# Optimization experiments

Measured on AMD Instinct MI355X. Metric: run time of the kernel, lower is better.

Reference implementation:

```python
import jax, jax.numpy as jnp
import numpy as np

HIDDEN = 4096
NUM_HEADS = 32
NUM_KV_HEADS = 8
HEAD_DIM = 128
T = 2048
ROPE_THETA = 10000.0


def setup_inputs() -> dict:
    key = jax.random.key(0)
    ks = jax.random.split(key, 10)
    s = 0.02
    return {
        "hidden_states": jax.random.normal(ks[0], (T, HIDDEN), dtype=jnp.float32),
        "positions": jnp.arange(T, dtype=jnp.int32),
        "Wq": jax.random.normal(ks[1], (NUM_HEADS * HEAD_DIM, HIDDEN), dtype=jnp.float32) * s,
        "bq": jax.random.normal(ks[2], (NUM_HEADS * HEAD_DIM,), dtype=jnp.float32) * s,
        "Wk": jax.random.normal(ks[3], (NUM_KV_HEADS * HEAD_DIM, HIDDEN), dtype=jnp.float32) * s,
        "bk": jax.random.normal(ks[4], (NUM_KV_HEADS * HEAD_DIM,), dtype=jnp.float32) * s,
        "Wv": jax.random.normal(ks[5], (NUM_KV_HEADS * HEAD_DIM, HIDDEN), dtype=jnp.float32) * s,
        "bv": jax.random.normal(ks[6], (NUM_KV_HEADS * HEAD_DIM,), dtype=jnp.float32) * s,
        "Wo": jax.random.normal(ks[7], (HIDDEN, HIDDEN), dtype=jnp.float32) * s,
        "bo": jax.random.normal(ks[8], (HIDDEN,), dtype=jnp.float32) * s,
    }


def _rope_cos_sin(positions, head_dim, base):
    # neox-style rotary over the full head_dim
    half = head_dim // 2
    inv_freq = 1.0 / (base ** (jnp.arange(0, half, dtype=jnp.float32) * 2.0 / head_dim))
    angles = positions.astype(jnp.float32)[:, None] * inv_freq[None, :]  # [T, half]
    return jnp.cos(angles), jnp.sin(angles)


def _apply_rope(x, cos, sin):
    # x: [T, H, D]; neox: split halves, rotate
    half = x.shape[-1] // 2
    x1, x2 = x[..., :half], x[..., half:]
    c = cos[:, None, :]
    s = sin[:, None, :]
    return jnp.concatenate([x1 * c - x2 * s, x2 * c + x1 * s], axis=-1)


def reference(hidden_states, positions, Wq, bq, Wk, bk, Wv, bv, Wo, bo):
    q = (hidden_states @ Wq.T + bq).reshape(T, NUM_HEADS, HEAD_DIM)
    k = (hidden_states @ Wk.T + bk).reshape(T, NUM_KV_HEADS, HEAD_DIM)
    v = (hidden_states @ Wv.T + bv).reshape(T, NUM_KV_HEADS, HEAD_DIM)

    cos, sin = _rope_cos_sin(positions, HEAD_DIM, ROPE_THETA)
    q = _apply_rope(q, cos, sin)
    k = _apply_rope(k, cos, sin)

    scale = 1.0 / np.sqrt(HEAD_DIM).astype(np.float32)
    group = NUM_HEADS // NUM_KV_HEADS
    qg = q.reshape(T, NUM_KV_HEADS, group, HEAD_DIM)
    # scores: [g_kv, r, q, k] without materializing repeated KV heads
    scores = jnp.einsum('qgrd,kgd->grqk', qg, k) * scale
    causal = positions[:, None] >= positions[None, :]  # [T, T]
    scores = jnp.where(causal[None, None], scores, jnp.finfo(scores.dtype).min)
    probs = jax.nn.softmax(scores, axis=-1)
    o = jnp.einsum('grqk,kgd->qgrd', probs, v).reshape(T, NUM_HEADS * HEAD_DIM)
    return o @ Wo.T + bo
```

## Files before the change

### kernel.cpp

```cpp
#include <hip/hip_runtime.h>
#include <stdint.h>

typedef unsigned short u16;
typedef __bf16 bf16x8_t __attribute__((ext_vector_type(8)));
typedef float f32x4_t __attribute__((ext_vector_type(4)));

#define T_SEQ 2048
#define HID 4096
#define ROWQKV 6144

__device__ __forceinline__ float bf2f(u16 x){ return __uint_as_float(((uint32_t)x)<<16); }
__device__ __forceinline__ u16 f2bf(float f){
  uint32_t u = __float_as_uint(f);
  return (u16)((u + 0x7fffu + ((u>>16)&1u)) >> 16);
}

__device__ __forceinline__ void gload16(const void* g, void* l){
  __builtin_amdgcn_global_load_lds(
      (const __attribute__((address_space(1))) uint32_t*)g,
      (__attribute__((address_space(3))) uint32_t*)l, 16, 0, 0);
}

__device__ __forceinline__ uint32_t cvtpk(float lo, float hi_){
  uint32_t r;
  asm("v_cvt_pk_bf16_f32 %0, %1, %2" : "=v"(r) : "v"(lo), "v"(hi_));
  return r;
}

__global__ void cvt_kernel(const float* __restrict__ src, u16* __restrict__ dst, int n8){
  int i = blockIdx.x*blockDim.x + threadIdx.x;
  if (i >= n8) return;
  const float4* s = (const float4*)src;
  float4 a = s[2*i], b = s[2*i+1];
  union { u16 u[8]; uint4 v; } o;
  o.u[0]=f2bf(a.x); o.u[1]=f2bf(a.y); o.u[2]=f2bf(a.z); o.u[3]=f2bf(a.w);
  o.u[4]=f2bf(b.x); o.u[5]=f2bf(b.y); o.u[6]=f2bf(b.z); o.u[7]=f2bf(b.w);
  ((uint4*)dst)[i] = o.v;
}

__global__ void setup_kernel(const float* __restrict__ bq, const float* __restrict__ bk,
                             const float* __restrict__ bv, const int* __restrict__ pos,
                             float* __restrict__ bqkv, float* __restrict__ cost,
                             float* __restrict__ sint){
  int i = blockIdx.x*blockDim.x + threadIdx.x;
  if (i < 6144) bqkv[i] = (i<4096) ? bq[i] : ((i<5120) ? bk[i-4096] : bv[i-5120]);
  if (i < T_SEQ*64){
    int t = i >> 6, d = i & 63;
    float inv = powf(10000.0f, -(float)(2*d) / 128.0f);
    float ang = (float)pos[t] * inv;
    cost[i] = cosf(ang);
    sint[i] = sinf(ang);
  }
}

#define GBAR __builtin_amdgcn_s_barrier()
#define LGKM0 do{ asm volatile("s_waitcnt lgkmcnt(0)" ::: "memory"); \
                  __builtin_amdgcn_sched_barrier(0); }while(0)

#define BUF6 28672

#define AREAD6(mh, ck) do{ \
  const u16* ab = &lds[cur + aoff + (mh)*4096]; \
  afr[0] = *(const bf16x8_t*)&ab[0*1024 + (ck)]; \
  afr[1] = *(const bf16x8_t*)&ab[1*1024 + (ck)]; \
  afr[2] = *(const bf16x8_t*)&ab[2*1024 + (ck)]; \
  afr[3] = *(const bf16x8_t*)&ab[3*1024 + (ck)]; }while(0)

#define BREAD6(ck) do{ \
  const u16* bb = &lds[cur + boff]; \
  bfr[0] = *(const bf16x8_t*)&bb[0*1024 + (ck)]; \
  bfr[1] = *(const bf16x8_t*)&bb[1*1024 + (ck)]; \
  bfr[2] = *(const bf16x8_t*)&bb[2*1024 + (ck)]; }while(0)

#define MM12(mh) do{ \
  _Pragma("unroll") \
  for (int mi=0; mi<4; ++mi){ \
    _Pragma("unroll") \
    for (int n=0; n<3; ++n) \
      acc[(mh)*4+mi][n] = __builtin_amdgcn_mfma_f32_16x16x32_bf16(afr[mi], bfr[n], acc[(mh)*4+mi][n],0,0,0); \
  } }while(0)

__global__ __launch_bounds__(512, 2)
void gemm_qkv(const u16* __restrict__ A, const u16* __restrict__ B,
              const float* __restrict__ bias, u16* __restrict__ Cb,
              int K, int N)
{
  __shared__ u16 lds[2*BUF6];
  const int tid = threadIdx.x, lane = tid & 63, w = tid >> 6;
  const int l15 = lane & 15, l4 = lane >> 4;
  const int wm = w >> 2, wn = w & 3;

  const int nwg = gridDim.x * gridDim.y;
  int flat = blockIdx.y * gridDim.x + blockIdx.x;
  flat = (flat & 7) * (nwg >> 3) + (flat >> 3);
  const int bx = flat % gridDim.x, by = flat / gridDim.x;
  const int bm = by * 256, bn = bx * 192;

  const int srow = w*8 + (lane >> 3);
  const int swc  = ((lane & 7) ^ (lane >> 3)) * 8;
  const u16* pA = A + (size_t)(bm + srow)*K + swc;
  const u16* pB = B + (size_t)(bn + srow)*K + swc;
  const size_t j64 = (size_t)64*K;
  const int wu = w*512;

  const int cA0 = ((0 + l4) ^ (l15 & 7)) * 8;
  const int cA1 = ((4 + l4) ^ (l15 & 7)) * 8;
  const int aoff = (wm*128 + l15) * 64;
  const int boff = 16384 + (wn*48 + l15) * 64;

  f32x4_t acc[8][3] = {};
  const int KT = K >> 6;

  gload16(pA + 0*j64, &lds[0     + wu]);
  gload16(pA + 1*j64, &lds[4096  + wu]);
  gload16(pA + 2*j64, &lds[8192  + wu]);
  gload16(pA + 3*j64, &lds[12288 + wu]);
  gload16(pB + 0*j64, &lds[16384 + wu]);
  gload16(pB + 1*j64, &lds[20480 + wu]);
  gload16(pB + 2*j64, &lds[24576 + wu]);
  pA += 64; pB += 64;
  asm volatile("s_waitcnt vmcnt(0)" ::: "memory");
  GBAR;

  for (int t = 0; t < KT; ++t){
    const int cur = (t & 1) * BUF6;
    const int nxt = ((t + 1) & 1) * BUF6;
    const bool st = (t + 1 < KT);
    bf16x8_t afr[4], bfr[3];

    BREAD6(cA0); AREAD6(0, cA0);
    if (st){
      gload16(pA + 0*j64, &lds[nxt + 0     + wu]);
      gload16(pA + 1*j64, &lds[nxt + 4096  + wu]);
      gload16(pA + 2*j64, &lds[nxt + 8192  + wu]);
      gload16(pA + 3*j64, &lds[nxt + 12288 + wu]);
    }
    GBAR; LGKM0;
    __builtin_amdgcn_s_setprio(1); MM12(0); __builtin_amdgcn_s_setprio(0);
    GBAR;

    AREAD6(1, cA0);
    if (st){
      gload16(pB + 0*j64, &lds[nxt + 16384 + wu]);
      gload16(pB + 1*j64, &lds[nxt + 20480 + wu]);
      gload16(pB + 2*j64, &lds[nxt + 24576 + wu]);
      pA += 64; pB += 64;
    }
    GBAR; LGKM0;
    __builtin_amdgcn_s_setprio(1); MM12(1); __builtin_amdgcn_s_setprio(0);
    GBAR;

    BREAD6(cA1); AREAD6(0, cA1);
    GBAR; LGKM0;
    __builtin_amdgcn_s_setprio(1); MM12(0); __builtin_amdgcn_s_setprio(0);
    GBAR;

    AREAD6(1, cA1);
    GBAR; LGKM0;
    __builtin_amdgcn_s_setprio(1); MM12(1); __builtin_amdgcn_s_setprio(0);
    if (st) asm volatile("s_waitcnt vmcnt(0)" ::: "memory");
    GBAR;
  }

  #pragma unroll
  for (int m=0;m<8;m++){
    #pragma unroll
    for (int n=0;n<3;n++){
      #pragma unroll
      for (int j=0;j<4;j++){
        int row = bm + wm*128 + (m>>2)*64 + (m&3)*16 + l4*4 + j;
        int col = bn + wn*48 + n*16 + l15;
        Cb[(size_t)row*N + col] = f2bf(acc[m][n][j] + bias[col]);
      }
    }
  }
}

#define BUFK 24576

#define KMREAD(ck) do{ \
  afr[0] = *(const bf16x8_t*)&lds[cur + aoff + 0*1024 + (ck)]; \
  afr[1] = *(const bf16x8_t*)&lds[cur + aoff + 1*1024 + (ck)]; \
  afr[2] = *(const bf16x8_t*)&lds[cur + aoff + 2*1024 + (ck)]; \
  afr[3] = *(const bf16x8_t*)&lds[cur + aoff + 3*1024 + (ck)]; \
  bfr[0] = *(const bf16x8_t*)&lds[cur + boff + 0*1024 + (ck)]; \
  bfr[1] = *(const bf16x8_t*)&lds[cur + boff + 1*1024 + (ck)]; \
  bfr[2] = *(const bf16x8_t*)&lds[cur + boff + 2*1024 + (ck)]; \
  bfr[3] = *(const bf16x8_t*)&lds[cur + boff + 3*1024 + (ck)]; }while(0)

#define MM16KM do{ \
  _Pragma("unroll") \
  for (int mi=0; mi<4; ++mi){ \
    _Pragma("unroll") \
    for (int n=0; n<4; ++n) \
      acc[mi][n] = __builtin_amdgcn_mfma_f32_16x16x32_bf16(afr[mi], bfr[n], acc[mi][n],0,0,0); \
  } }while(0)

__global__ __launch_bounds__(512, 2)
void gemm_km(const u16* __restrict__ A, const u16* __restrict__ B,
             const float* __restrict__ bias, float* __restrict__ Cf,
             int K, int N)
{
  __shared__ u16 lds[3*BUFK];
  const int tid = threadIdx.x, lane = tid & 63, w = tid >> 6;
  const int l15 = lane & 15, l4 = lane >> 4;
  const int wm = w >> 1, wn = w & 1;

  const int nwg = gridDim.x * gridDim.y;
  int flat = blockIdx.y * gridDim.x + blockIdx.x;
  flat = (flat & 7) * (nwg >> 3) + (flat >> 3);
  const int bx = flat % gridDim.x, by = flat / gridDim.x;
  const int bm = by * 256, bn = bx * 128;

  const int srow = w*8 + (lane >> 3);
  const int swc  = ((lane & 7) ^ (lane >> 3)) * 8;
  const u16* pA = A + (size_t)(bm + srow)*K + swc;
  const u16* pB = B + (size_t)(bn + srow)*K + swc;
  const size_t j64 = (size_t)64*K;
  const int wu = w*512;

  const int cA0 = ((0 + l4) ^ (l15 & 7)) * 8;
  const int cA1 = ((4 + l4) ^ (l15 & 7)) * 8;
  const int aoff = (wm*64 + l15) * 64;
  const int boff = 16384 + (wn*64 + l15) * 64;

  f32x4_t acc[4][4] = {};
  const int KT = K >> 6;

  gload16(pA + 0*j64,      &lds[0*4096 + wu]);
  gload16(pA + 1*j64,      &lds[1*4096 + wu]);
  gload16(pA + 2*j64,      &lds[2*4096 + wu]);
  gload16(pA + 3*j64,      &lds[3*4096 + wu]);
  gload16(pB + 0*j64,      &lds[16384 + 0*4096 + wu]);
  gload16(pB + 1*j64,      &lds[16384 + 1*4096 + wu]);
  gload16(pA + 64 + 0*j64, &lds[BUFK + 0*4096 + wu]);
  gload16(pA + 64 + 1*j64, &lds[BUFK + 1*4096 + wu]);
  gload16(pA + 64 + 2*j64, &lds[BUFK + 2*4096 + wu]);
  gload16(pA + 64 + 3*j64, &lds[BUFK + 3*4096 + wu]);
  gload16(pB + 64 + 0*j64, &lds[BUFK + 16384 + 0*4096 + wu]);
  gload16(pB + 64 + 1*j64, &lds[BUFK + 16384 + 1*4096 + wu]);
  pA += 128; pB += 128;
  asm volatile("s_waitcnt vmcnt(6)" ::: "memory");
  GBAR;

  for (int t = 0; t < KT; ++t){
    const int cur = (t % 3) * BUFK;
    const int sb  = ((t + 2) % 3) * BUFK;
    const bool st = (t + 2 < KT);
    bf16x8_t afr[4], bfr[4];

    KMREAD(cA0);
    if (st){
      gload16(pA + 0*j64, &lds[sb + 0*4096 + wu]);
      gload16(pA + 1*j64, &lds[sb + 1*4096 + wu]);
      gload16(pA + 2*j64, &lds[sb + 2*4096 + wu]);
    }
    GBAR; LGKM0;
    __builtin_amdgcn_s_setprio(1); MM16KM; __builtin_amdgcn_s_setprio(0);
    GBAR;

    KMREAD(cA1);
    if (st){
      gload16(pA + 3*j64, &lds[sb + 3*4096 + wu]);
      gload16(pB + 0*j64, &lds[sb + 16384 + 0*4096 + wu]);
      gload16(pB + 1*j64, &lds[sb + 16384 + 1*4096 + wu]);
      pA += 64; pB += 64;
    }
    GBAR; LGKM0;
    __builtin_amdgcn_s_setprio(1); MM16KM; __builtin_amdgcn_s_setprio(0);
    if (st)              asm volatile("s_waitcnt vmcnt(6)" ::: "memory");
    else if (t + 1 < KT) asm volatile("s_waitcnt vmcnt(0)" ::: "memory");
    GBAR;
  }

  #pragma unroll
  for (int mi=0;mi<4;mi++){
    #pragma unroll
    for (int n=0;n<4;n++){
      #pragma unroll
      for (int j=0;j<4;j++){
        int row = bm + wm*64 + mi*16 + l4*4 + j;
        int col = bn + wn*64 + n*16 + l15;
        Cf[(size_t)row*N + col] = acc[mi][n][j] + bias[col];
      }
    }
  }
}

__global__ void rope_kernel(u16* __restrict__ qkv, const float* __restrict__ cost,
                            const float* __restrict__ sint){
  int i = blockIdx.x*blockDim.x + threadIdx.x;
  int t = i / 2560;
  int r = i % 2560;
  int h = r >> 6, d = r & 63;
  int base = (h < 32) ? h*128 : (4096 + (h-32)*128);
  size_t p1 = (size_t)t*ROWQKV + base + d;
  float x1 = bf2f(qkv[p1]), x2 = bf2f(qkv[p1+64]);
  float c = cost[(t<<6)+d], s = sint[(t<<6)+d];
  qkv[p1]    = f2bf(x1*c - x2*s);
  qkv[p1+64] = f2bf(x2*c + x1*s);
}

#define VOFF 16384
#define POFF 25600

__global__ __launch_bounds__(256, 2)
void attn_kernel(const u16* __restrict__ qkv, u16* __restrict__ attn_o)
{
  __shared__ u16 lds[29696];
  const int tid = threadIdx.x, lane = tid&63, wid = tid>>6;
  const int l15 = lane&15, l4 = lane>>4;
  const int l7 = l15 & 7;
  const int h  = blockIdx.x & 31;
  const int qt = 31 - (blockIdx.x >> 5);
  const int q0 = qt * 64;
  const int kvh = h >> 2;
  const u16* Qg = qkv + h*128;
  const u16* Kg = qkv + 4096 + kvh*128;
  const u16* Vg = qkv + 5120 + kvh*128;
  const float c2 = 0.127543147f;

  bf16x8_t qf[4];
  {
    size_t qrow = (size_t)(q0 + wid*16 + l15);
    #pragma unroll
    for (int kk=0;kk<4;kk++)
      qf[kk] = *(const bf16x8_t*)(Qg + qrow*ROWQKV + kk*32 + l4*8);
  }
  float mrow[4] = {-1e30f,-1e30f,-1e30f,-1e30f};
  f32x4_t oacc[9] = {};

  const u16* ksrc[4];
  int kls[4];
  #pragma unroll
  for (int i=0;i<4;i++){
    const int c = wid*4 + i;
    ksrc[i] = Kg + (size_t)((c&7)*8 + (lane>>3))*ROWQKV
               + (c>>3)*64 + ((lane&7)^(lane>>3))*8;
    kls[i] = c*512;
  }
  const int kvp = tid & 31;
  const int vd0 = (tid >> 5) * 16;
  uint4 rv[4];

  #pragma unroll
  for (int i=0;i<4;i++) gload16(ksrc[i], &lds[kls[i]]);
  #pragma unroll
  for (int i=0;i<4;i++) ksrc[i] += (size_t)64*ROWQKV;
  {
    const u16* va = Vg + (size_t)(2*kvp)*ROWQKV + vd0;
    rv[0] = *(const uint4*)va;            rv[1] = *(const uint4*)(va + 8);
    rv[2] = *(const uint4*)(va + ROWQKV); rv[3] = *(const uint4*)(va + ROWQKV + 8);
    *(uint32_t*)&lds[24576 + tid*4]     = 0x3F803F80u;
    *(uint32_t*)&lds[24576 + tid*4 + 2] = 0x3F803F80u;
  }
  __syncthreads();
  {
    const u16* ra = (const u16*)&rv[0]; const u16* rb = (const u16*)&rv[2];
    #pragma unroll
    for (int e=0;e<8;e++)
      *(uint32_t*)&lds[VOFF + (vd0+e)*64 + ((kvp>>2)^(e&7))*8 + 2*(kvp&3)]
          = (uint32_t)ra[e] | ((uint32_t)rb[e] << 16);
    ra = (const u16*)&rv[1]; rb = (const u16*)&rv[3];
    #pragma unroll
    for (int e=0;e<8;e++)
      *(uint32_t*)&lds[VOFF + (vd0+8+e)*64 + ((kvp>>2)^(e&7))*8 + 2*(kvp&3)]
          = (uint32_t)ra[e] | ((uint32_t)rb[e] << 16);
  }
  __syncthreads();

  for (int kt = 0; kt <= qt; ++kt){
    const int kv0 = kt * 64;
    const int kcur = (kt & 1) * 8192;
    const bool pre = (kt < qt);
    if (pre){
      const int knxt = ((kt+1) & 1) * 8192;
      #pragma unroll
      for (int i=0;i<4;i++) gload16(ksrc[i], &lds[knxt + kls[i]]);
      #pragma unroll
      for (int i=0;i<4;i++) ksrc[i] += (size_t)64*ROWQKV;
      const u16* va = Vg + (size_t)(kv0 + 64 + 2*kvp)*ROWQKV + vd0;
      rv[0] = *(const uint4*)va;            rv[1] = *(const uint4*)(va + 8);
      rv[2] = *(const uint4*)(va + ROWQKV); rv[3] = *(const uint4*)(va + ROWQKV + 8);
    }

    f32x4_t sacc[4] = {};
    __builtin_amdgcn_s_setprio(1);
    #pragma unroll
    for (int n=0;n<4;n++){
      #pragma unroll
      for (int kk=0;kk<4;kk++){
        bf16x8_t kf = *(const bf16x8_t*)&lds[kcur + (kk>>1)*4096
                        + (n*16+l15)*64 + (((kk&1)*4 + l4) ^ l7)*8];
        sacc[n] = __builtin_amdgcn_mfma_f32_16x16x32_bf16(qf[kk], kf, sacc[n], 0,0,0);
      }
    }
    __builtin_amdgcn_s_setprio(0);
    float sv[4][4];
    float pmax[4] = {-1e30f,-1e30f,-1e30f,-1e30f};
    bool diag = (kt == qt);
    #pragma unroll
    for (int n=0;n<4;n++){
      int kvcol = kv0 + n*16 + l15;
      #pragma unroll
      for (int j=0;j<4;j++){
        float s = sacc[n][j];
        int qrow = q0 + wid*16 + l4*4 + j;
        if (diag && kvcol > qrow) s = -1e30f;
        sv[n][j] = s;
        pmax[j] = fmaxf(pmax[j], s);
      }
    }
    #pragma unroll
    for (int off=1; off<16; off<<=1){
      #pragma unroll
      for (int j=0;j<4;j++)
        pmax[j] = fmaxf(pmax[j], __shfl_xor(pmax[j], off, 64));
    }
    float esc[4], mc[4];
    #pragma unroll
    for (int j=0;j<4;j++){
      float mn = fmaxf(mrow[j], pmax[j]);
      esc[j] = exp2f((mrow[j] - mn) * c2);
      mrow[j] = mn;
      mc[j] = mn * c2;
    }
    #pragma unroll
    for (int n=0;n<4;n++){
      #pragma unroll
      for (int j=0;j<4;j++)
        sv[n][j] = exp2f(fmaf(sv[n][j], c2, -mc[j]));
    }
    #pragma unroll
    for (int n=0;n<9;n++){
      #pragma unroll
      for (int j=0;j<4;j++) oacc[n][j] *= esc[j];
    }
    {
      const int r0 = wid*16 + l4*4;
      #pragma unroll
      for (int n=0;n<4;n++){
        uint32_t p01 = cvtpk(sv[n][0], sv[n][1]);
        uint32_t p23 = cvtpk(sv[n][2], sv[n][3]);
        const int cb = n*2 + (l15>>3);
        lds[POFF + (r0+0)*64 + ((cb ^ ((r0+0)&7))*8) + l7] = (u16)p01;
        lds[POFF + (r0+1)*64 + ((cb ^ ((r0+1)&7))*8) + l7] = (u16)(p01 >> 16);
        lds[POFF + (r0+2)*64 + ((cb ^ ((r0+2)&7))*8) + l7] = (u16)p23;
        lds[POFF + (r0+3)*64 + ((cb ^ ((r0+3)&7))*8) + l7] = (u16)(p23 >> 16);
      }
    }
    __builtin_amdgcn_s_setprio(1);
    #pragma unroll
    for (int kk=0;kk<2;kk++){
      const int blk = ((kk*4 + l4) ^ l7)*8;
      bf16x8_t pf = *(const bf16x8_t*)&lds[POFF + (wid*16 + l15)*64 + blk];
      #pragma unroll
      for (int n=0;n<9;n++){
        bf16x8_t vf = *(const bf16x8_t*)&lds[VOFF + (n*16 + l15)*64 + blk];
        oacc[n] = __builtin_amdgcn_mfma_f32_16x16x32_bf16(pf, vf, oacc[n], 0,0,0);
      }
    }
    __builtin_amdgcn_s_setprio(0);
    __syncthreads();
    if (pre){
      const u16* ra = (const u16*)&rv[0]; const u16* rb = (const u16*)&rv[2];
      #pragma unroll
      for (int e=0;e<8;e++)
        *(uint32_t*)&lds[VOFF + (vd0+e)*64 + ((kvp>>2)^(e&7))*8 + 2*(kvp&3)]
            = (uint32_t)ra[e] | ((uint32_t)rb[e] << 16);
      ra = (const u16*)&rv[1]; rb = (const u16*)&rv[3];
      #pragma unroll
      for (int e=0;e<8;e++)
        *(uint32_t*)&lds[VOFF + (vd0+8+e)*64 + ((kvp>>2)^(e&7))*8 + 2*(kvp&3)]
            = (uint32_t)ra[e] | ((uint32_t)rb[e] << 16);
    }
    __syncthreads();
  }

  {
    float inv[4];
    #pragma unroll
    for (int j=0;j<4;j++) inv[j] = 1.0f / oacc[8][j];
    #pragma unroll
    for (int n=0;n<8;n++){
      #pragma unroll
      for (int j=0;j<4;j++){
        int qrow = q0 + wid*16 + l4*4 + j;
        int col  = h*128 + n*16 + l15;
        attn_o[(size_t)qrow*HID + col] = f2bf(oacc[n][j] * inv[j]);
      }
    }
  }
}

extern "C" void kernel_launch(void* const* d_in, const int* in_sizes, int n_in,
                              void* d_out, int out_size, void* d_ws, size_t ws_size,
                              hipStream_t stream)
{
  const float* hs = (const float*)d_in[0];
  const int*  pos = (const int*)d_in[1];
  const float* Wq = (const float*)d_in[2];
  const float* bq = (const float*)d_in[3];
  const float* Wk = (const float*)d_in[4];
  const float* bk = (const float*)d_in[5];
  const float* Wv = (const float*)d_in[6];
  const float* bv = (const float*)d_in[7];
  const float* Wo = (const float*)d_in[8];
  const float* bo = (const float*)d_in[9];
  float* out = (float*)d_out;

  char* ws = (char*)d_ws;
  u16* hs_bf   = (u16*)ws;  ws += (size_t)2048*4096*2;
  u16* Wqkv_bf = (u16*)ws;  ws += (size_t)6144*4096*2;
  u16* Wo_bf   = (u16*)ws;  ws += (size_t)4096*4096*2;
  u16* qkv     = (u16*)ws;  ws += (size_t)2048*6144*2;
  u16* attn_b  = (u16*)ws;  ws += (size_t)2048*4096*2;
  float* bqkv  = (float*)ws; ws += (size_t)6144*4;
  float* cost  = (float*)ws; ws += (size_t)2048*64*4;
  float* sint  = (float*)ws; ws += (size_t)2048*64*4;

  {
    int n8 = 2048*4096/8;
    cvt_kernel<<<(n8+255)/256, 256, 0, stream>>>(hs, hs_bf, n8);
    n8 = 4096*4096/8;
    cvt_kernel<<<(n8+255)/256, 256, 0, stream>>>(Wq, Wqkv_bf, n8);
    n8 = 1024*4096/8;
    cvt_kernel<<<(n8+255)/256, 256, 0, stream>>>(Wk, Wqkv_bf + (size_t)4096*4096, n8);
    cvt_kernel<<<(n8+255)/256, 256, 0, stream>>>(Wv, Wqkv_bf + (size_t)5120*4096, n8);
    n8 = 4096*4096/8;
    cvt_kernel<<<(n8+255)/256, 256, 0, stream>>>(Wo, Wo_bf, n8);
  }
  setup_kernel<<<(T_SEQ*64 + 255)/256, 256, 0, stream>>>(bq, bk, bv, pos, bqkv, cost, sint);

  gemm_qkv<<<dim3(6144/192, 2048/256), 512, 0, stream>>>(hs_bf, Wqkv_bf, bqkv, qkv, 4096, 6144);
  rope_kernel<<<(T_SEQ*40*64)/256, 256, 0, stream>>>(qkv, cost, sint);
  attn_kernel<<<1024, 256, 0, stream>>>(qkv, attn_b);
  gemm_km<<<dim3(4096/128, 2048/256), 512, 0, stream>>>(attn_b, Wo_bf, bo, out, 4096, 4096);
}
```

Measured before the change: 333.3 us.

## Fuse fp32-to-bf16 weight conversion into GEMM B-operand loads

Drops the separate conversion kernels for Wq/Wk/Wv/Wo. Each GEMM now reads fp32 weights into registers, packs them to bf16, and writes them to LDS. This removes a full read and write pass over the weights. The cost is that each weight tile is now read once per M-block in fp32, doubling the bytes per load, and the register-staged path replaces the async global_load_lds path. It also cuts gemm_km from triple to double buffering.

```diff
diff --git a/kernel.cpp b/kernel.cpp
--- a/kernel.cpp
+++ b/kernel.cpp
@@ -80,8 +80,20 @@
       acc[(mh)*4+mi][n] = __builtin_amdgcn_mfma_f32_16x16x32_bf16(afr[mi], bfr[n], acc[(mh)*4+mi][n],0,0,0); \
   } }while(0)
 
+#define BCVT3(dstbase) do{ \
+  _Pragma("unroll") \
+  for (int c=0;c<3;c++){ \
+    union { u16 u[8]; uint4 v; } ob; \
+    *(uint32_t*)&ob.u[0] = cvtpk(rb[c][0].x, rb[c][0].y); \
+    *(uint32_t*)&ob.u[2] = cvtpk(rb[c][0].z, rb[c][0].w); \
+    *(uint32_t*)&ob.u[4] = cvtpk(rb[c][1].x, rb[c][1].y); \
+    *(uint32_t*)&ob.u[6] = cvtpk(rb[c][1].z, rb[c][1].w); \
+    *(uint4*)&lds[(dstbase) + 16384 + c*4096 + wu + lane*8] = ob.v; \
+  } }while(0)
+
 __global__ __launch_bounds__(512, 2)
-void gemm_qkv(const u16* __restrict__ A, const u16* __restrict__ B,
+void gemm_qkv(const u16* __restrict__ A, const float* __restrict__ Wq,
+              const float* __restrict__ Wk, const float* __restrict__ Wv,
               const float* __restrict__ bias, u16* __restrict__ Cb,
               int K, int N)
 {
@@ -99,9 +111,18 @@
   const int srow = w*8 + (lane >> 3);
   const int swc  = ((lane & 7) ^ (lane >> 3)) * 8;
   const u16* pA = A + (size_t)(bm + srow)*K + swc;
-  const u16* pB = B + (size_t)(bn + srow)*K + swc;
   const size_t j64 = (size_t)64*K;
   const int wu = w*512;
+
+  const float* pBf[3];
+  #pragma unroll
+  for (int c=0;c<3;c++){
+    int r = bn + c*64 + srow;
+    const float* base = (r < 4096) ? (Wq + (size_t)r*K)
+                      : (r < 5120) ? (Wk + (size_t)(r-4096)*K)
+                                   : (Wv + (size_t)(r-5120)*K);
+    pBf[c] = base + swc;
+  }
 
   const int cA0 = ((0 + l4) ^ (l15 & 7)) * 8;
   const int cA1 = ((4 + l4) ^ (l15 & 7)) * 8;
@@ -115,10 +136,18 @@
   gload16(pA + 1*j64, &lds[4096  + wu]);
   gload16(pA + 2*j64, &lds[8192  + wu]);
   gload16(pA + 3*j64, &lds[12288 + wu]);
-  gload16(pB + 0*j64, &lds[16384 + wu]);
-  gload16(pB + 1*j64, &lds[20480 + wu]);
-  gload16(pB + 2*j64, &lds[24576 + wu]);
-  pA += 64; pB += 64;
+  {
+    float4 rb[3][2];
+    #pragma unroll
+    for (int c=0;c<3;c++){
+      rb[c][0] = *(const float4*)(pBf[c]);
+      rb[c][1] = *(const float4*)(pBf[c] + 4);
+    }
+    BCVT3(0);
+    #pragma unroll
+    for (int c=0;c<3;c++) pBf[c] += 64;
+  }
+  pA += 64;
   asm volatile("s_waitcnt vmcnt(0)" ::: "memory");
   GBAR;
 
@@ -127,6 +156,7 @@
     const int nxt = ((t + 1) & 1) * BUF6;
     const bool st = (t + 1 < KT);
     bf16x8_t afr[4], bfr[3];
+    float4 rb[3][2];
 
     BREAD6(cA0); AREAD6(0, cA0);
     if (st){
@@ -141,16 +171,23 @@
 
     AREAD6(1, cA0);
     if (st){
-      gload16(pB + 0*j64, &lds[nxt + 16384 + wu]);
-      gload16(pB + 1*j64, &lds[nxt + 20480 + wu]);
-      gload16(pB + 2*j64, &lds[nxt + 24576 + wu]);
-      pA += 64; pB += 64;
+      #pragma unroll
+      for (int c=0;c<3;c++){
+        rb[c][0] = *(const float4*)(pBf[c]);
+        rb[c][1] = *(const float4*)(pBf[c] + 4);
+      }
     }
     GBAR; LGKM0;
     __builtin_amdgcn_s_setprio(1); MM12(1); __builtin_amdgcn_s_setprio(0);
     GBAR;
 
     BREAD6(cA1); AREAD6(0, cA1);
+    if (st){
+      BCVT3(nxt);
+      #pragma unroll
+      for (int c=0;c<3;c++) pBf[c] += 64;
+      pA += 64;
+    }
     GBAR; LGKM0;
     __builtin_amdgcn_s_setprio(1); MM12(0); __builtin_amdgcn_s_setprio(0);
     GBAR;
@@ -176,7 +213,7 @@
   }
 }
 
-#define BUFK 24576
+#define BUFK2 24576
 
 #define KMREAD(ck) do{ \
   afr[0] = *(const bf16x8_t*)&lds[cur + aoff + 0*1024 + (ck)]; \
@@ -196,12 +233,23 @@
       acc[mi][n] = __builtin_amdgcn_mfma_f32_16x16x32_bf16(afr[mi], bfr[n], acc[mi][n],0,0,0); \
   } }while(0)
 
+#define BCVT2(dstbase) do{ \
+  _Pragma("unroll") \
+  for (int c=0;c<2;c++){ \
+    union { u16 u[8]; uint4 v; } ob; \
+    *(uint32_t*)&ob.u[0] = cvtpk(rb[c][0].x, rb[c][0].y); \
+    *(uint32_t*)&ob.u[2] = cvtpk(rb[c][0].z, rb[c][0].w); \
+    *(uint32_t*)&ob.u[4] = cvtpk(rb[c][1].x, rb[c][1].y); \
+    *(uint32_t*)&ob.u[6] = cvtpk(rb[c][1].z, rb[c][1].w); \
+    *(uint4*)&lds[(dstbase) + 16384 + c*4096 + wu + lane*8] = ob.v; \
+  } }while(0)
+
 __global__ __launch_bounds__(512, 2)
-void gemm_km(const u16* __restrict__ A, const u16* __restrict__ B,
+void gemm_km(const u16* __restrict__ A, const float* __restrict__ Wo,
              const float* __restrict__ bias, float* __restrict__ Cf,
              int K, int N)
 {
-  __shared__ u16 lds[3*BUFK];
+  __shared__ u16 lds[2*BUFK2];
   const int tid = threadIdx.x, lane = tid & 63, w = tid >> 6;
   const int l15 = lane & 15, l4 = lane >> 4;
   const int wm = w >> 1, wn = w & 1;
@@ -215,9 +263,13 @@
   const int srow = w*8 + (lane >> 3);
   const int swc  = ((lane & 7) ^ (lane >> 3)) * 8;
   const u16* pA = A + (size_t)(bm + srow)*K + swc;
-  const u16* pB = B + (size_t)(bn + srow)*K + swc;
   const size_t j64 = (size_t)64*K;
   const int wu = w*512;
+
+  const float* pBf[2];
+  #pragma unroll
+  for (int c=0;c<2;c++)
+    pBf[c] = Wo + (size_t)(bn + c*64 + srow)*K + swc;
 
   const int cA0 = ((0 + l4) ^ (l15 & 7)) * 8;
   const int cA1 = ((4 + l4) ^ (l15 & 7)) * 8;
@@ -227,33 +279,43 @@
   f32x4_t acc[4][4] = {};
   const int KT = K >> 6;
 
-  gload16(pA + 0*j64,      &lds[0*4096 + wu]);
-  gload16(pA + 1*j64,      &lds[1*4096 + wu]);
-  gload16(pA + 2*j64,      &lds[2*4096 + wu]);
-  gload16(pA + 3*j64,      &lds[3*4096 + wu]);
-  gload16(pB + 0*j64,      &lds[16384 + 0*4096 + wu]);
-  gload16(pB + 1*j64,      &lds[16384 + 1*4096 + wu]);
-  gload16(pA + 64 + 0*j64, &lds[BUFK + 0*4096 + wu]);
-  gload16(pA + 64 + 1*j64, &lds[BUFK + 1*4096 + wu]);
-  gload16(pA + 64 + 2*j64, &lds[BUFK + 2*4096 + wu]);
-  gload16(pA + 64 + 3*j64, &lds[BUFK + 3*4096 + wu]);
-  gload16(pB + 64 + 0*j64, &lds[BUFK + 16384 + 0*4096 + wu]);
-  gload16(pB + 64 + 1*j64, &lds[BUFK + 16384 + 1*4096 + wu]);
-  pA += 128; pB += 128;
-  asm volatile("s_waitcnt vmcnt(6)" ::: "memory");
+  gload16(pA + 0*j64, &lds[0*4096 + wu]);
+  gload16(pA + 1*j64, &lds[1*4096 + wu]);
+  gload16(pA + 2*j64, &lds[2*4096 + wu]);
+  gload16(pA + 3*j64, &lds[3*4096 + wu]);
+  {
+    float4 rb[2][2];
+    #pragma unroll
+    for (int c=0;c<2;c++){
+      rb[c][0] = *(const float4*)(pBf[c]);
+      rb[c][1] = *(const float4*)(pBf[c] + 4);
+    }
+    BCVT2(0);
+    #pragma unroll
+    for (int c=0;c<2;c++) pBf[c] += 64;
+  }
+  pA += 64;
+  asm volatile("s_waitcnt vmcnt(0)" ::: "memory");
   GBAR;
 
   for (int t = 0; t < KT; ++t){
-    const int cur = (t % 3) * BUFK;
-    const int sb  = ((t + 2) % 3) * BUFK;
-    const bool st = (t + 2 < KT);
+    const int cur = (t & 1) * BUFK2;
+    const int nxt = ((t + 1) & 1) * BUFK2;
+    const bool st = (t + 1 < KT);
     bf16x8_t afr[4], bfr[4];
+    float4 rb[2][2];
 
     KMREAD(cA0);
     if (st){
-      gload16(pA + 0*j64, &lds[sb + 0*4096 + wu]);
-      gload16(pA + 1*j64, &lds[sb + 1*4096 + wu]);
-      gload16(pA + 2*j64, &lds[sb + 2*4096 + wu]);
+      gload16(pA + 0*j64, &lds[nxt + 0*4096 + wu]);
+      gload16(pA + 1*j64, &lds[nxt + 1*4096 + wu]);
+      gload16(pA + 2*j64, &lds[nxt + 2*4096 + wu]);
+      gload16(pA + 3*j64, &lds[nxt + 3*4096 + wu]);
+      #pragma unroll
+      for (int c=0;c<2;c++){
+        rb[c][0] = *(const float4*)(pBf[c]);
+        rb[c][1] = *(const float4*)(pBf[c] + 4);
+      }
     }
     GBAR; LGKM0;
     __builtin_amdgcn_s_setprio(1); MM16KM; __builtin_amdgcn_s_setprio(0);
@@ -261,15 +323,14 @@
 
     KMREAD(cA1);
     if (st){
-      gload16(pA + 3*j64, &lds[sb + 3*4096 + wu]);
-      gload16(pB + 0*j64, &lds[sb + 16384 + 0*4096 + wu]);
-      gload16(pB + 1*j64, &lds[sb + 16384 + 1*4096 + wu]);
-      pA += 64; pB += 64;
+      BCVT2(nxt);
+      #pragma unroll
+      for (int c=0;c<2;c++) pBf[c] += 64;
+      pA += 64;
     }
     GBAR; LGKM0;
     __builtin_amdgcn_s_setprio(1); MM16KM; __builtin_amdgcn_s_setprio(0);
-    if (st)              asm volatile("s_waitcnt vmcnt(6)" ::: "memory");
-    else if (t + 1 < KT) asm volatile("s_waitcnt vmcnt(0)" ::: "memory");
+    if (st) asm volatile("s_waitcnt vmcnt(0)" ::: "memory");
     GBAR;
   }
 
@@ -511,8 +572,6 @@
 
   char* ws = (char*)d_ws;
   u16* hs_bf   = (u16*)ws;  ws += (size_t)2048*4096*2;
-  u16* Wqkv_bf = (u16*)ws;  ws += (size_t)6144*4096*2;
-  u16* Wo_bf   = (u16*)ws;  ws += (size_t)4096*4096*2;
   u16* qkv     = (u16*)ws;  ws += (size_t)2048*6144*2;
   u16* attn_b  = (u16*)ws;  ws += (size_t)2048*4096*2;
   float* bqkv  = (float*)ws; ws += (size_t)6144*4;
@@ -522,18 +581,11 @@
   {
     int n8 = 2048*4096/8;
     cvt_kernel<<<(n8+255)/256, 256, 0, stream>>>(hs, hs_bf, n8);
-    n8 = 4096*4096/8;
-    cvt_kernel<<<(n8+255)/256, 256, 0, stream>>>(Wq, Wqkv_bf, n8);
-    n8 = 1024*4096/8;
-    cvt_kernel<<<(n8+255)/256, 256, 0, stream>>>(Wk, Wqkv_bf + (size_t)4096*4096, n8);
-    cvt_kernel<<<(n8+255)/256, 256, 0, stream>>>(Wv, Wqkv_bf + (size_t)5120*4096, n8);
-    n8 = 4096*4096/8;
-    cvt_kernel<<<(n8+255)/256, 256, 0, stream>>>(Wo, Wo_bf, n8);
   }
   setup_kernel<<<(T_SEQ*64 + 255)/256, 256, 0, stream>>>(bq, bk, bv, pos, bqkv, cost, sint);
 
-  gemm_qkv<<<dim3(6144/192, 2048/256), 512, 0, stream>>>(hs_bf, Wqkv_bf, bqkv, qkv, 4096, 6144);
+  gemm_qkv<<<dim3(6144/192, 2048/256), 512, 0, stream>>>(hs_bf, Wq, Wk, Wv, bqkv, qkv, 4096, 6144);
   rope_kernel<<<(T_SEQ*40*64)/256, 256, 0, stream>>>(qkv, cost, sint);
   attn_kernel<<<1024, 256, 0, stream>>>(qkv, attn_b);
-  gemm_km<<<dim3(4096/128, 2048/256), 512, 0, stream>>>(attn_b, Wo_bf, bo, out, 4096, 4096);
-}
+  gemm_km<<<dim3(4096/128, 2048/256), 512, 0, stream>>>(attn_b, Wo, bo, out, 4096, 4096);
+}
```

Measured after the change: 382.3 us. 14.7% more time.
